# Kernel tuning notes

Measured on AMD Instinct MI355X. Metric: run time of the kernel, lower is better.

The kernel has to match this reference:

```python
import jax, jax.numpy as jnp
import numpy as np

NUM_HEADS = 4

def setup_inputs() -> dict:
    key = jax.random.key(0)
    ks = jax.random.split(key, 8)
    B, C, H, W = 4, 256, 128, 128
    Cq = C // 8  # query/key channels
    x  = jax.random.normal(ks[0], (B, C, H, W), dtype=jnp.float32)
    Wq = jax.random.normal(ks[1], (Cq, C), dtype=jnp.float32) * 0.05
    bq = jax.random.normal(ks[2], (Cq,),  dtype=jnp.float32) * 0.01
    Wk = jax.random.normal(ks[3], (Cq, C), dtype=jnp.float32) * 0.05
    bk = jax.random.normal(ks[4], (Cq,),  dtype=jnp.float32) * 0.01
    Wv = jax.random.normal(ks[5], (C, C),  dtype=jnp.float32) * 0.05
    bv = jax.random.normal(ks[6], (C,),   dtype=jnp.float32) * 0.01
    # torch init is zeros; use a nonzero value so the attention path contributes
    gamma = jnp.array([0.5], dtype=jnp.float32)
    return {"x": x, "Wq": Wq, "bq": bq, "Wk": Wk, "bk": bk, "Wv": Wv, "bv": bv, "gamma": gamma}

def _conv1x1(x, Wm, b):
    # 1x1 conv == per-pixel linear map over channels
    return jnp.einsum('bchw,oc->bohw', x, Wm) + b[None, :, None, None]

def reference(x, Wq, bq, Wk, bk, Wv, bv, gamma):
    B, C, H, W = x.shape
    nh = NUM_HEADS
    # project, then fold heads into batch: (B*nh, c_head, H, W)
    q = _conv1x1(x, Wq, bq).reshape(B * nh, -1, H, W)
    k = _conv1x1(x, Wk, bk).reshape(B * nh, -1, H, W)
    v = _conv1x1(x, Wv, bv).reshape(B * nh, -1, H, W)
    # horizontal (row-wise) attention over W: energy [BH, H, W, W]
    e_h = jnp.einsum('bchw,bchv->bhwv', q, k)
    a_h = jax.nn.softmax(e_h, axis=-1)
    o_h = jnp.einsum('bhwv,bchv->bchw', a_h, v)  # (BH, cv, H, W)
    # vertical (column-wise) attention over H: energy [BH, W, H, H]
    e_v = jnp.einsum('bchw,bcgw->bwhg', q, k)
    a_v = jax.nn.softmax(e_v, axis=-1)
    # original permutes back as (BH, cv, W, H); requires H == W to add
    o_v = jnp.einsum('bwhg,bcgw->bcwh', a_v, v)
    attn = (o_h + o_v).reshape(B, C, H, W)
    return gamma * attn + x
```

## Files before the change

kernel.cpp:

```cpp
#include <hip/hip_runtime.h>

#define HW 16384

typedef __attribute__((ext_vector_type(8))) short short8;
typedef __attribute__((ext_vector_type(16))) float floatx16;
typedef __attribute__((ext_vector_type(4))) unsigned int uvec4;

__device__ inline unsigned short f2bf(float f) {
    unsigned u = __builtin_bit_cast(unsigned, f);
    u = (u + 0x7FFFu + ((u >> 16) & 1u)) >> 16;
    return (unsigned short)u;
}

__device__ inline unsigned pack_bf_trunc(float lo, float hi) {
    return __builtin_amdgcn_perm(__builtin_bit_cast(unsigned, hi),
                                 __builtin_bit_cast(unsigned, lo), 0x07060302u);
}

__global__ __launch_bounds__(256) void castW_kernel(
    const float* __restrict__ Wq, const float* __restrict__ Wk,
    const float* __restrict__ Wv, unsigned short* __restrict__ Wb)
{
    int idx4 = blockIdx.x * 256 + threadIdx.x;
    int e0 = idx4 * 4;
    int row = e0 >> 8, col = e0 & 255;
    const float* src = (row < 32) ? (Wq + row * 256 + col)
                     : (row < 64) ? (Wk + (row - 32) * 256 + col)
                                  : (Wv + (row - 64) * 256 + col);
    float4 v = *(const float4*)src;
    uint2 pk;
    pk.x = f2bf(v.x) | ((unsigned)f2bf(v.y) << 16);
    pk.y = f2bf(v.z) | ((unsigned)f2bf(v.w) << 16);
    *(uint2*)&Wb[e0] = pk;
}

__global__ __launch_bounds__(256) void cast_xt_kernel(
    const float* __restrict__ x, unsigned short* __restrict__ xt)
{
    __shared__ unsigned short T[64][66];
    const int tid = threadIdx.x;
    const int p0 = blockIdx.x * 64;
    const int c0 = blockIdx.y * 64;
    const int b  = blockIdx.z;
    #pragma unroll
    for (int i = 0; i < 4; i++) {
        int e = i * 256 + tid;
        int c = e >> 4, seg = e & 15;
        float4 v = *(const float4*)&x[((b * 256 + c0 + c) << 14) + p0 + seg * 4];
        ((unsigned*)&T[c][seg * 4])[0] = f2bf(v.x) | ((unsigned)f2bf(v.y) << 16);
        ((unsigned*)&T[c][seg * 4])[1] = f2bf(v.z) | ((unsigned)f2bf(v.w) << 16);
    }
    __syncthreads();
    #pragma unroll
    for (int i = 0; i < 2; i++) {
        int e = i * 256 + tid;
        int p = e >> 3, cs = e & 7;
        unsigned short t[8];
        #pragma unroll
        for (int j = 0; j < 8; j++) t[j] = T[cs * 8 + j][p];
        uint4 pk;
        pk.x = t[0] | ((unsigned)t[1] << 16);
        pk.y = t[2] | ((unsigned)t[3] << 16);
        pk.z = t[4] | ((unsigned)t[5] << 16);
        pk.w = t[6] | ((unsigned)t[7] << 16);
        *(uint4*)&xt[(((b << 14) + p0 + p) << 8) + c0 + cs * 8] = pk;
    }
}

__global__ __launch_bounds__(256, 3) void proj_mfma_kernel(
    const unsigned short* __restrict__ Wb, const unsigned short* __restrict__ xt,
    const float* __restrict__ bq, const float* __restrict__ bk,
    const float* __restrict__ bv,
    unsigned short* __restrict__ qb, unsigned short* __restrict__ kb,
    unsigned short* __restrict__ vb)
{
    __shared__ __align__(16) unsigned short As[64 * 64];
    __shared__ __align__(16) unsigned short Bs[256 * 64];
    __shared__ float biasS[64];
    const int tid = threadIdx.x;
    const int p0  = blockIdx.x * 256;
    const int oc0 = blockIdx.y * 64;
    const int b   = blockIdx.z;
    const int w = tid >> 6, lr = tid & 31, lh = (tid & 63) >> 5;

    if (tid < 64) biasS[tid] = (oc0 == 0) ? ((tid < 32) ? bq[tid] : bk[tid - 32])
                                          : bv[oc0 - 64 + tid];

    floatx16 z16 = {0,0,0,0,0,0,0,0,0,0,0,0,0,0,0,0};
    floatx16 acc[2][2] = {{z16, z16}, {z16, z16}};
    const int bpx = (b << 14) + p0;

    for (int kc = 0; kc < 256; kc += 64) {
        if (kc) __syncthreads();
        #pragma unroll
        for (int i = 0; i < 2; i++) {
            int e = i * 256 + tid;
            int row = e >> 3, seg = e & 7, cp = seg ^ (row & 7);
            *(uint4*)&As[row * 64 + cp * 8] =
                *(const uint4*)&Wb[(oc0 + row) * 256 + kc + seg * 8];
        }
        #pragma unroll
        for (int i = 0; i < 8; i++) {
            int e = i * 256 + tid;
            int row = e >> 3, seg = e & 7, cp = seg ^ (row & 7);
            *(uint4*)&Bs[row * 64 + cp * 8] =
                *(const uint4*)&xt[((bpx + row) << 8) + kc + seg * 8];
        }
        __syncthreads();
        #pragma unroll
        for (int ks = 0; ks < 4; ks++) {
            int c = 2 * ks + lh;
            int cx = (c ^ (lr & 7)) * 8;
            short8 af0 = *(const short8*)&As[lr * 64 + cx];
            short8 af1 = *(const short8*)&As[(32 + lr) * 64 + cx];
            short8 bf0 = *(const short8*)&Bs[(64 * w + lr) * 64 + cx];
            short8 bf1 = *(const short8*)&Bs[(64 * w + 32 + lr) * 64 + cx];
            acc[0][0] = __builtin_amdgcn_mfma_f32_32x32x16_bf16(af0, bf0, acc[0][0], 0, 0, 0);
            acc[0][1] = __builtin_amdgcn_mfma_f32_32x32x16_bf16(af0, bf1, acc[0][1], 0, 0, 0);
            acc[1][0] = __builtin_amdgcn_mfma_f32_32x32x16_bf16(af1, bf0, acc[1][0], 0, 0, 0);
            acc[1][1] = __builtin_amdgcn_mfma_f32_32x32x16_bf16(af1, bf1, acc[1][1], 0, 0, 0);
        }
    }

    __syncthreads();
    if (oc0 == 0) {
        unsigned short* Cq = Bs;
        #pragma unroll
        for (int i = 0; i < 2; i++) {
            #pragma unroll
            for (int j = 0; j < 2; j++) {
                int px = 64 * w + 32 * j + lr;
                #pragma unroll
                for (int g = 0; g < 4; g++) {
                    float v0 = acc[i][j][4*g+0] + biasS[32*i + 8*g + 4*lh + 0];
                    float v1 = acc[i][j][4*g+1] + biasS[32*i + 8*g + 4*lh + 1];
                    float v2 = acc[i][j][4*g+2] + biasS[32*i + 8*g + 4*lh + 2];
                    float v3 = acc[i][j][4*g+3] + biasS[32*i + 8*g + 4*lh + 3];
                    uint2 u; u.x = pack_bf_trunc(v0, v1); u.y = pack_bf_trunc(v2, v3);
                    int cp = (4 * i + g) ^ (px & 7);
                    *(uint2*)&Cq[px * 64 + cp * 8 + 4 * lh] = u;
                }
            }
        }
        __syncthreads();
        #pragma unroll
        for (int i = 0; i < 8; i++) {
            int px = tid;
            int cp = i ^ (px & 7);
            uint4 val = *(const uint4*)&Cq[px * 64 + cp * 8];
            if (i < 4) *(uint4*)&qb[(unsigned)((b * 4 + i)     * HW + p0 + px) * 8] = val;
            else       *(uint4*)&kb[(unsigned)((b * 4 + i - 4) * HW + p0 + px) * 8] = val;
        }
    } else {
        unsigned short* Cv = Bs;
        #pragma unroll
        for (int i = 0; i < 2; i++) {
            #pragma unroll
            for (int j = 0; j < 2; j++) {
                int px = 64 * w + 32 * j + lr;
                #pragma unroll
                for (int reg = 0; reg < 16; reg++) {
                    int oc = 32 * i + (reg & 3) + 8 * (reg >> 2) + 4 * lh;
                    float v = acc[i][j][reg] + biasS[oc];
                    int cp = (px >> 3) ^ (oc & 31);
                    Cv[oc * 256 + cp * 8 + (px & 7)] =
                        (unsigned short)(__builtin_bit_cast(unsigned, v) >> 16);
                }
            }
        }
        __syncthreads();
        #pragma unroll
        for (int i = 0; i < 8; i++) {
            int u = i * 256 + tid;
            int oc = u >> 5, seg = u & 31;
            int cp = seg ^ (oc & 31);
            uint4 val = *(const uint4*)&Cv[oc * 256 + cp * 8];
            *(uint4*)&vb[(unsigned)(b * 256 + oc0 - 64 + oc) * HW + p0 + seg * 8] = val;
        }
    }
}

__global__ __launch_bounds__(256) void tqk_kernel(
    const unsigned short* __restrict__ qb, const unsigned short* __restrict__ kb,
    unsigned short* __restrict__ qt, unsigned short* __restrict__ kt)
{
    __shared__ uint4 t[32][33];
    const int plane = blockIdx.y;
    const int tile  = blockIdx.x;
    const int tx = tile & 3, ty = tile >> 2;
    const uint4* src = (const uint4*)(plane < 16 ? qb : kb) + (plane & 15) * HW;
    uint4*       dst = (uint4*)(plane < 16 ? qt : kt) + (plane & 15) * HW;
    const int c = threadIdx.x & 31, r0 = threadIdx.x >> 5;
    #pragma unroll
    for (int i = 0; i < 4; i++) {
        int r = r0 + i * 8;
        t[r][c] = src[(ty * 32 + r) * 128 + tx * 32 + c];
    }
    __syncthreads();
    #pragma unroll
    for (int i = 0; i < 4; i++) {
        int r = r0 + i * 8;
        dst[(tx * 32 + r) * 128 + ty * 32 + c] = t[c][r];
    }
}

__global__ __launch_bounds__(256) void tv_kernel(
    const unsigned short* __restrict__ vb, unsigned short* __restrict__ vt)
{
    __shared__ unsigned short T[64][66];
    const int plane = blockIdx.y;
    const int tile  = blockIdx.x;
    const int tx = tile & 1, ty = tile >> 1;
    const unsigned* src = (const unsigned*)(vb + plane * HW);
    unsigned*       dst = (unsigned*)(vt + plane * HW);
    const int tid = threadIdx.x;
    #pragma unroll
    for (int i = 0; i < 8; i++) {
        int e = i * 256 + tid;
        int r = e >> 5, cp = e & 31;
        *(unsigned*)&T[r][2 * cp] = src[(ty * 64 + r) * 64 + tx * 32 + cp];
    }
    __syncthreads();
    #pragma unroll
    for (int i = 0; i < 8; i++) {
        int e = i * 256 + tid;
        int c = e >> 5, rp = e & 31;
        unsigned lo = T[2 * rp][c], hi = T[2 * rp + 1][c];
        dst[(tx * 64 + c) * 64 + ty * 32 + rp] = lo | (hi << 16);
    }
}

__global__ __launch_bounds__(256, 2) void attn_kernel(
    const unsigned short* __restrict__ qb, const unsigned short* __restrict__ kb,
    const unsigned short* __restrict__ vb,
    const unsigned short* __restrict__ qt, const unsigned short* __restrict__ kt,
    const unsigned short* __restrict__ vt,
    const float* __restrict__ xin, const float* __restrict__ gamma,
    float* __restrict__ out)
{
    __shared__ __align__(16) unsigned short Vs[2][64 * 128];

    const int tid = threadIdx.x;
    const int y = blockIdx.x, bh = blockIdx.y;
    const int w = tid >> 6, l = tid & 63, lr = l & 31, lh = l >> 5;
    const float L2E = 1.4426950408889634f;

    #pragma unroll
    for (int s = 0; s < 2; s++) {
        const unsigned short* vsrc = s ? vt : vb;
        #pragma unroll
        for (int i = 0; i < 4; i++) {
            int e = i * 256 + tid;
            int ch = e >> 4, sg = e & 15, sgp = sg ^ (ch & 15);
            *(uint4*)&Vs[s][ch * 128 + sgp * 8] =
                *(const uint4*)(vsrc + (bh * 64 + ch) * HW + y * 128 + sg * 8);
        }
    }
    __syncthreads();

    floatx16 z16 = {0,0,0,0,0,0,0,0,0,0,0,0,0,0,0,0};
    floatx16 o0 = z16, o1 = z16;
    short8 z8 = {0,0,0,0,0,0,0,0};
    float s0s = 1.0f;

    #pragma unroll
    for (int stage = 0; stage < 2; stage++) {
        const unsigned short* qsrc = (stage ? qt : qb) + (bh * 128 + y) * 1024;
        const unsigned short* ksrc = (stage ? kt : kb) + (bh * 128 + y) * 1024;
        short8 bf = z8;
        if (lh == 0) bf = *(const short8*)(qsrc + (32 * w + lr) * 8);

        float partial = 0.f;
        short8 pf[8];
        #pragma unroll
        for (int kg = 0; kg < 4; kg++) {
            short8 af = z8;
            if (lh == 0) af = *(const short8*)(ksrc + (32 * kg + lr) * 8);
            floatx16 e = __builtin_amdgcn_mfma_f32_32x32x16_bf16(af, bf, z16, 0, 0, 0);
            #pragma unroll
            for (int r = 0; r < 16; r++) {
                float p = exp2f(e[r] * L2E);
                e[r] = p;
                partial += p;
            }
            #pragma unroll
            for (int cc = 0; cc < 2; cc++) {
                unsigned X0 = pack_bf_trunc(e[8*cc+0], e[8*cc+1]);
                unsigned X1 = pack_bf_trunc(e[8*cc+2], e[8*cc+3]);
                unsigned X2 = pack_bf_trunc(e[8*cc+4], e[8*cc+5]);
                unsigned X3 = pack_bf_trunc(e[8*cc+6], e[8*cc+7]);
                unsigned pX0 = __shfl_xor(X0, 32);
                unsigned pX1 = __shfl_xor(X1, 32);
                unsigned pX2 = __shfl_xor(X2, 32);
                unsigned pX3 = __shfl_xor(X3, 32);
                uvec4 t;
                t.x = lh ? pX2 : X0;
                t.y = lh ? pX3 : X1;
                t.z = lh ? X2  : pX0;
                t.w = lh ? X3  : pX1;
                pf[2 * kg + cc] = __builtin_bit_cast(short8, t);
            }
        }
        float ssum = partial + __shfl_xor(partial, 32);
        if (stage == 1) {
            float f = ssum / s0s;
            #pragma unroll
            for (int r = 0; r < 16; r++) { o0[r] *= f; o1[r] *= f; }
        }
        s0s = ssum;

        #pragma unroll
        for (int ks = 0; ks < 8; ks++) {
            int cp = ((2 * ks + lh) ^ (lr & 15)) * 8;
            short8 v0 = *(const short8*)&Vs[stage][lr * 128 + cp];
            short8 v1 = *(const short8*)&Vs[stage][(32 + lr) * 128 + cp];
            o0 = __builtin_amdgcn_mfma_f32_32x32x16_bf16(v0, pf[ks], o0, 0, 0, 0);
            o1 = __builtin_amdgcn_mfma_f32_32x32x16_bf16(v1, pf[ks], o1, 0, 0, 0);
        }
    }

    __syncthreads();

    const float gs = gamma[0] / s0s;
    const int xq = 32 * w + lr;
    #pragma unroll
    for (int reg = 0; reg < 16; reg++) {
        int ch = (reg & 3) + 8 * (reg >> 2) + 4 * lh;
        int idx0 = (bh * 64 + ch) * HW + y * 128 + xq;
        int idx1 = (bh * 64 + 32 + ch) * HW + y * 128 + xq;
        out[idx0] = gs * o0[reg] + xin[idx0];
        out[idx1] = gs * o1[reg] + xin[idx1];
    }
}

extern "C" void kernel_launch(void* const* d_in, const int* in_sizes, int n_in,
                              void* d_out, int out_size, void* d_ws, size_t ws_size,
                              hipStream_t stream) {
    const float* x     = (const float*)d_in[0];
    const float* Wq    = (const float*)d_in[1];
    const float* bq    = (const float*)d_in[2];
    const float* Wk    = (const float*)d_in[3];
    const float* bk    = (const float*)d_in[4];
    const float* Wv    = (const float*)d_in[5];
    const float* bv    = (const float*)d_in[6];
    const float* gamma = (const float*)d_in[7];
    float* out = (float*)d_out;

    unsigned short* Wb   = (unsigned short*)d_ws;
    unsigned short* qb16 = Wb + 320 * 256;
    unsigned short* kb16 = qb16 + 16 * HW * 8;
    unsigned short* qt16 = kb16 + 16 * HW * 8;
    unsigned short* kt16 = qt16 + 16 * HW * 8;
    unsigned short* vb16 = kt16 + 16 * HW * 8;
    unsigned short* vt16 = vb16 + 1024 * HW;
    unsigned short* xt = (unsigned short*)d_out;

    castW_kernel<<<dim3(80), 256, 0, stream>>>(Wq, Wk, Wv, Wb);
    cast_xt_kernel<<<dim3(256, 4, 4), 256, 0, stream>>>(x, xt);
    proj_mfma_kernel<<<dim3(64, 5, 4), 256, 0, stream>>>(Wb, xt, bq, bk, bv, qb16, kb16, vb16);
    tqk_kernel<<<dim3(16, 32), 256, 0, stream>>>(qb16, kb16, qt16, kt16);
    tv_kernel<<<dim3(4, 1024), 256, 0, stream>>>(vb16, vt16);
    attn_kernel<<<dim3(128, 16), 256, 0, stream>>>(qb16, kb16, vb16, qt16, kt16, vt16, x, gamma, out);
}
```

Measured before the change: 201.2 us.

## Fold weight cast into x cast, prescale Q by log2e, split attention accumulators

Merges the weight cast kernel into the x transpose/cast kernel to remove one launch. The log2(e) factor is folded into the Q weights and bias, which removes a multiply per exponent in the attention kernel. The attention kernel now keeps separate horizontal and vertical accumulators and issues the PV MFMAs interleaved with the exp/pack work instead of rescaling between stages, each normalized at the end. This costs more accumulator registers, and rounding Q weights to bf16 after scaling slightly changes precision.

Measured after the change: 198.9 us. No clear change (-1.1%).

```diff
diff --git a/kernel.cpp b/kernel.cpp
--- a/kernel.cpp
+++ b/kernel.cpp
@@ -17,31 +17,35 @@
                                  __builtin_bit_cast(unsigned, lo), 0x07060302u);
 }
 
-__global__ __launch_bounds__(256) void castW_kernel(
+__global__ __launch_bounds__(256) void cast_xt_kernel(
+    const float* __restrict__ x,
     const float* __restrict__ Wq, const float* __restrict__ Wk,
-    const float* __restrict__ Wv, unsigned short* __restrict__ Wb)
-{
-    int idx4 = blockIdx.x * 256 + threadIdx.x;
-    int e0 = idx4 * 4;
-    int row = e0 >> 8, col = e0 & 255;
-    const float* src = (row < 32) ? (Wq + row * 256 + col)
-                     : (row < 64) ? (Wk + (row - 32) * 256 + col)
-                                  : (Wv + (row - 64) * 256 + col);
-    float4 v = *(const float4*)src;
-    uint2 pk;
-    pk.x = f2bf(v.x) | ((unsigned)f2bf(v.y) << 16);
-    pk.y = f2bf(v.z) | ((unsigned)f2bf(v.w) << 16);
-    *(uint2*)&Wb[e0] = pk;
-}
-
-__global__ __launch_bounds__(256) void cast_xt_kernel(
-    const float* __restrict__ x, unsigned short* __restrict__ xt)
+    const float* __restrict__ Wv, unsigned short* __restrict__ Wb,
+    unsigned short* __restrict__ xt)
 {
     __shared__ unsigned short T[64][66];
     const int tid = threadIdx.x;
     const int p0 = blockIdx.x * 64;
     const int c0 = blockIdx.y * 64;
     const int b  = blockIdx.z;
+
+    if (b == 0 && blockIdx.y == 0 && blockIdx.x < 80) {
+        int e0 = (blockIdx.x * 256 + tid) * 4;
+        int row = e0 >> 8, col = e0 & 255;
+        const float* src = (row < 32) ? (Wq + row * 256 + col)
+                         : (row < 64) ? (Wk + (row - 32) * 256 + col)
+                                      : (Wv + (row - 64) * 256 + col);
+        float4 v = *(const float4*)src;
+        if (row < 32) {
+            const float L2E = 1.4426950408889634f;
+            v.x *= L2E; v.y *= L2E; v.z *= L2E; v.w *= L2E;
+        }
+        uint2 pk;
+        pk.x = f2bf(v.x) | ((unsigned)f2bf(v.y) << 16);
+        pk.y = f2bf(v.z) | ((unsigned)f2bf(v.w) << 16);
+        *(uint2*)&Wb[e0] = pk;
+    }
+
     #pragma unroll
     for (int i = 0; i < 4; i++) {
         int e = i * 256 + tid;
@@ -83,8 +87,9 @@
     const int b   = blockIdx.z;
     const int w = tid >> 6, lr = tid & 31, lh = (tid & 63) >> 5;
 
-    if (tid < 64) biasS[tid] = (oc0 == 0) ? ((tid < 32) ? bq[tid] : bk[tid - 32])
-                                          : bv[oc0 - 64 + tid];
+    if (tid < 64) biasS[tid] = (oc0 == 0)
+        ? ((tid < 32) ? bq[tid] * 1.4426950408889634f : bk[tid - 32])
+        : bv[oc0 - 64 + tid];
 
     floatx16 z16 = {0,0,0,0,0,0,0,0,0,0,0,0,0,0,0,0};
     floatx16 acc[2][2] = {{z16, z16}, {z16, z16}};
@@ -243,7 +248,6 @@
     const int tid = threadIdx.x;
     const int y = blockIdx.x, bh = blockIdx.y;
     const int w = tid >> 6, l = tid & 63, lr = l & 31, lh = l >> 5;
-    const float L2E = 1.4426950408889634f;
 
     #pragma unroll
     for (int s = 0; s < 2; s++) {
@@ -259,9 +263,10 @@
     __syncthreads();
 
     floatx16 z16 = {0,0,0,0,0,0,0,0,0,0,0,0,0,0,0,0};
-    floatx16 o0 = z16, o1 = z16;
+    floatx16 oh0 = z16, oh1 = z16;
+    floatx16 ov0 = z16, ov1 = z16;
     short8 z8 = {0,0,0,0,0,0,0,0};
-    float s0s = 1.0f;
+    float ssA = 1.0f, ssB = 1.0f;
 
     #pragma unroll
     for (int stage = 0; stage < 2; stage++) {
@@ -270,16 +275,21 @@
         short8 bf = z8;
         if (lh == 0) bf = *(const short8*)(qsrc + (32 * w + lr) * 8);
 
-        float partial = 0.f;
-        short8 pf[8];
+        floatx16 et[4];
         #pragma unroll
         for (int kg = 0; kg < 4; kg++) {
             short8 af = z8;
             if (lh == 0) af = *(const short8*)(ksrc + (32 * kg + lr) * 8);
-            floatx16 e = __builtin_amdgcn_mfma_f32_32x32x16_bf16(af, bf, z16, 0, 0, 0);
+            et[kg] = __builtin_amdgcn_mfma_f32_32x32x16_bf16(af, bf, z16, 0, 0, 0);
+        }
+
+        float partial = 0.f;
+        #pragma unroll
+        for (int kg = 0; kg < 4; kg++) {
+            floatx16 e = et[kg];
             #pragma unroll
             for (int r = 0; r < 16; r++) {
-                float p = exp2f(e[r] * L2E);
+                float p = exp2f(e[r]);
                 e[r] = p;
                 partial += p;
             }
@@ -298,38 +308,36 @@
                 t.y = lh ? pX3 : X1;
                 t.z = lh ? X2  : pX0;
                 t.w = lh ? X3  : pX1;
-                pf[2 * kg + cc] = __builtin_bit_cast(short8, t);
+                short8 pf = __builtin_bit_cast(short8, t);
+                int ks = 2 * kg + cc;
+                int cp = ((2 * ks + lh) ^ (lr & 15)) * 8;
+                short8 v0 = *(const short8*)&Vs[stage][lr * 128 + cp];
+                short8 v1 = *(const short8*)&Vs[stage][(32 + lr) * 128 + cp];
+                if (stage == 0) {
+                    oh0 = __builtin_amdgcn_mfma_f32_32x32x16_bf16(v0, pf, oh0, 0, 0, 0);
+                    oh1 = __builtin_amdgcn_mfma_f32_32x32x16_bf16(v1, pf, oh1, 0, 0, 0);
+                } else {
+                    ov0 = __builtin_amdgcn_mfma_f32_32x32x16_bf16(v0, pf, ov0, 0, 0, 0);
+                    ov1 = __builtin_amdgcn_mfma_f32_32x32x16_bf16(v1, pf, ov1, 0, 0, 0);
+                }
             }
         }
         float ssum = partial + __shfl_xor(partial, 32);
-        if (stage == 1) {
-            float f = ssum / s0s;
-            #pragma unroll
-            for (int r = 0; r < 16; r++) { o0[r] *= f; o1[r] *= f; }
-        }
-        s0s = ssum;
-
-        #pragma unroll
-        for (int ks = 0; ks < 8; ks++) {
-            int cp = ((2 * ks + lh) ^ (lr & 15)) * 8;
-            short8 v0 = *(const short8*)&Vs[stage][lr * 128 + cp];
-            short8 v1 = *(const short8*)&Vs[stage][(32 + lr) * 128 + cp];
-            o0 = __builtin_amdgcn_mfma_f32_32x32x16_bf16(v0, pf[ks], o0, 0, 0, 0);
-            o1 = __builtin_amdgcn_mfma_f32_32x32x16_bf16(v1, pf[ks], o1, 0, 0, 0);
-        }
-    }
-
-    __syncthreads();
-
-    const float gs = gamma[0] / s0s;
+        if (stage == 0) ssA = ssum; else ssB = ssum;
+    }
+
+    __syncthreads();
+
+    const float g  = gamma[0];
+    const float g0 = g / ssA, g1 = g / ssB;
     const int xq = 32 * w + lr;
     #pragma unroll
     for (int reg = 0; reg < 16; reg++) {
         int ch = (reg & 3) + 8 * (reg >> 2) + 4 * lh;
         int idx0 = (bh * 64 + ch) * HW + y * 128 + xq;
         int idx1 = (bh * 64 + 32 + ch) * HW + y * 128 + xq;
-        out[idx0] = gs * o0[reg] + xin[idx0];
-        out[idx1] = gs * o1[reg] + xin[idx1];
+        out[idx0] = g0 * oh0[reg] + g1 * ov0[reg] + xin[idx0];
+        out[idx1] = g0 * oh1[reg] + g1 * ov1[reg] + xin[idx1];
     }
 }
 
@@ -355,8 +363,7 @@
     unsigned short* vt16 = vb16 + 1024 * HW;
     unsigned short* xt = (unsigned short*)d_out;
 
-    castW_kernel<<<dim3(80), 256, 0, stream>>>(Wq, Wk, Wv, Wb);
-    cast_xt_kernel<<<dim3(256, 4, 4), 256, 0, stream>>>(x, xt);
+    cast_xt_kernel<<<dim3(256, 4, 4), 256, 0, stream>>>(x, Wq, Wk, Wv, Wb, xt);
     proj_mfma_kernel<<<dim3(64, 5, 4), 256, 0, stream>>>(Wb, xt, bq, bk, bv, qb16, kb16, vb16);
     tqk_kernel<<<dim3(16, 32), 256, 0, stream>>>(qb16, kb16, qt16, kt16);
     tv_kernel<<<dim3(4, 1024), 256, 0, stream>>>(vb16, vt16);
```
